# Kernel optimization log

Measured on AMD Instinct MI355X. Metric: run time of the kernel, lower is better.

## Reference

```python
import jax, jax.numpy as jnp
import numpy as np

B, T, E = 4, 2_000_000, 8
C, K, STRIDE = 128, 512, 512
CHUNK, OVERLAP = 64000, 511  # overlap defaults to kernel_size - 1


def _candidate_positions(T):
    """Exact set of window start positions visited by the chunked streaming max.

    Replays the chunk loop of _lowmem_max_over_time: chunk starts advance by
    step = chunk_size - overlap (not a multiple of stride!), and within each
    chunk conv windows start at chunk_start + stride*k.
    """
    step = max(1, CHUNK - OVERLAP)
    pos = []
    start = 0
    while start < T:
        end = min(start + CHUNK, T)
        end_ext = min(end + OVERLAP, T)
        L = end_ext - start
        if L >= K:
            n = (L - K) // STRIDE + 1
            pos.append(start + STRIDE * np.arange(n, dtype=np.int64))
        if end == T:
            break
        start += step
    p = np.unique(np.concatenate(pos))
    return np.clip(p, 0, max(0, T - K))


POS = _candidate_positions(T)                       # [P] static window starts
WIN_IDX = POS[:, None] + np.arange(K, dtype=np.int64)  # [P, K] gather indices


def setup_inputs() -> dict:
    key = jax.random.key(0)
    ks = jax.random.split(key, 5)
    scale = 1.0 / float(np.sqrt(E * K))  # torch Conv1d default init range
    return {
        "x": jax.random.normal(ks[0], (B, T, E), dtype=jnp.float32),
        "w1": jax.random.uniform(ks[1], (C, E, K), jnp.float32, -scale, scale),
        "b1": jax.random.uniform(ks[2], (C,), jnp.float32, -scale, scale),
        "w2": jax.random.uniform(ks[3], (C, E, K), jnp.float32, -scale, scale),
        "b2": jax.random.uniform(ks[4], (C,), jnp.float32, -scale, scale),
    }


def reference(x, w1, b1, w2, b2):
    # Gather every candidate window the chunked scan would see: [B, P, K, E]
    wins = x[:, WIN_IDX, :]
    # Original clones windows under no_grad (stop_grad_input=True): input gets no grad.
    wins = jax.lax.stop_gradient(wins)
    # Gated conv (GLU): conv1(z) * sigmoid(conv2(z)) at each window -> [B, C, P]
    c1 = jnp.einsum('bpke,cek->bcp', wins, w1) + b1[:, None]
    c2 = jnp.einsum('bpke,cek->bcp', wins, w2) + b2[:, None]
    g = c1 * jax.nn.sigmoid(c2)
    # Global max-over-time per (batch, channel); identical value to the
    # running-max pass followed by exact re-evaluation at argmax positions.
    return g.max(axis=-1)  # [B, C]
```

## Files before the change

kernel.cpp:

```cpp
#include <hip/hip_runtime.h>


#define T_LEN 2000000
#define P_CNT 3937
#define M_TOT 15748
#define KD    4096

typedef __attribute__((ext_vector_type(8))) short short8;
typedef __attribute__((ext_vector_type(4))) float f32x4;

static __device__ __forceinline__ unsigned short f2bf(float f) {
    unsigned u = __builtin_bit_cast(unsigned, f);
    unsigned r = (u + 0x7FFFu + ((u >> 16) & 1u)) >> 16;
    return (unsigned short)r;
}

static __device__ __forceinline__ unsigned ordenc(float f) {
    unsigned u = __builtin_bit_cast(unsigned, f);
    return (u & 0x80000000u) ? ~u : (u | 0x80000000u);
}

static __device__ __forceinline__ size_t row_base_bp(int bb, int p) {
    int j, kp;
    if (p < 3875) { j = p / 125; kp = p - j * 125; }
    else          { j = 31;      kp = p - 3875; }
    long pos = (long)j * 63489 + (long)kp * 512;
    return ((size_t)bb * T_LEN + (size_t)pos) * 8u;
}

static __device__ __forceinline__ uint2 cvt4(float4 v) {
    unsigned lo, hi;
    asm("v_cvt_pk_bf16_f32 %0, %1, %2" : "=v"(lo) : "v"(v.x), "v"(v.y));
    asm("v_cvt_pk_bf16_f32 %0, %1, %2" : "=v"(hi) : "v"(v.z), "v"(v.w));
    uint2 u; u.x = lo; u.y = hi;
    return u;
}

__global__ __launch_bounds__(256) void pack_w(const float* __restrict__ w1,
                                              const float* __restrict__ w2,
                                              uint4* __restrict__ Bpf,
                                              unsigned* __restrict__ outu) {
    int c = blockIdx.x * 256 + threadIdx.x;
    if (c < 512) outu[c] = 0u;
    if (c >= 131072) return;
    int l  = c & 63;
    int w  = (c >> 6) & 15;
    int kq = (c >> 10) & 1;
    int ks = c >> 11;
    int cl = l & 15;
    int n  = (cl < 8) ? (w * 8 + cl) : (128 + w * 8 + (cl - 8));
    int kb = ks * 64 + kq * 32 + ((l >> 4) << 3);
    const float* src = (n < 128) ? w1 : w2;
    int cc = n & 127;
    unsigned short h[8];
#pragma unroll
    for (int j = 0; j < 8; ++j) {
        int k = kb + j;
        h[j] = f2bf(src[cc * 4096 + (k & 7) * 512 + (k >> 3)]);
    }
    uint4 v;
    v.x = (unsigned)h[0] | ((unsigned)h[1] << 16);
    v.y = (unsigned)h[2] | ((unsigned)h[3] << 16);
    v.z = (unsigned)h[4] | ((unsigned)h[5] << 16);
    v.w = (unsigned)h[6] | ((unsigned)h[7] << 16);
    Bpf[c] = v;
}

#define LOAD_B(BB, KS)                                                         \
    do {                                                                       \
        _Pragma("unroll")                                                      \
        for (int kq = 0; kq < 2; ++kq)                                         \
            BB[kq] = Bq[((KS) * 2 + kq) * 1024 + bbase];                       \
    } while (0)

#define STEP_NB(KS, BCUR, BNXT)                                                \
    do {                                                                       \
        const int ks_ = (KS);                                                  \
        const int ksn = (ks_ + 1 < 64) ? ks_ + 1 : 63;                         \
        LOAD_B(BNXT, ksn);                                                     \
        const int ksl = (ks_ + 6 < 64) ? ks_ + 6 : 63;                         \
        float4 aF = *(const float4*)(x + aoff + (size_t)(ksl * 64));           \
        const char* As = smem + (ks_ & 7) * 8192;                              \
        _Pragma("unroll")                                                      \
        for (int kq = 0; kq < 2; ++kq) {                                       \
            short8 b = __builtin_bit_cast(short8, BCUR[kq]);                   \
            _Pragma("unroll")                                                  \
            for (int mf = 0; mf < 4; ++mf) {                                   \
                short8 af = *(const short8*)(As + aro[kq][mf]);                \
                acc[mf] = __builtin_amdgcn_mfma_f32_16x16x32_bf16(             \
                    af, b, acc[mf], 0, 0, 0);                                  \
            }                                                                  \
        }                                                                      \
        if (ks_ + 4 < 64)                                                      \
            *(uint2*)(smem + ((ks_ + 4) & 7) * 8192 + awb) = cvt4(aA);         \
        aA = aB; aB = aF;                                                      \
    } while (0)

__global__ __launch_bounds__(1024, 4) void gemm_max(const float* __restrict__ x,
                                                    const uint4* __restrict__ Bq,
                                                    const float* __restrict__ b1,
                                                    const float* __restrict__ b2,
                                                    unsigned* __restrict__ outu) {
    __shared__ __align__(16) char smem[65536];

    const int t    = threadIdx.x;
    const int lane = t & 63;
    const int w    = t >> 6;
    const int bid  = blockIdx.x;
    const int bb   = bid / 62;
    const int p0   = (bid % 62) * 64;

    const int rowS = t >> 4;
    const int kcS  = t & 15;
    int pS = p0 + rowS; if (pS > P_CNT - 1) pS = P_CNT - 1;
    const size_t aoff = row_base_bp(bb, pS) + (size_t)(kcS * 4);
    const int    awb  = (rowS * 128 + kcS * 8) ^ ((rowS & 7) << 4);

    int aro[2][4];
#pragma unroll
    for (int kq = 0; kq < 2; ++kq)
#pragma unroll
        for (int mf = 0; mf < 4; ++mf) {
            int row = mf * 16 + (lane & 15);
            aro[kq][mf] = (row * 128 + kq * 64 + (lane >> 4) * 16)
                          ^ ((row & 7) << 4);
        }

    const int bbase = w * 64 + lane;

#pragma unroll
    for (int pt = 0; pt < 4; ++pt) {
        float4 v = *(const float4*)(x + aoff + pt * 64);
        *(uint2*)(smem + pt * 8192 + awb) = cvt4(v);
    }
    __syncthreads();

    float4 aA = *(const float4*)(x + aoff + 256);
    float4 aB = *(const float4*)(x + aoff + 320);
    uint4 BX[2], BY[2];
    LOAD_B(BX, 0);

    f32x4 acc[4];
#pragma unroll
    for (int mf = 0; mf < 4; ++mf) acc[mf] = (f32x4){0.f, 0.f, 0.f, 0.f};

    for (int ks = 0; ks < 64; ks += 2) {
        STEP_NB(ks, BX, BY);
        STEP_NB(ks + 1, BY, BX);
        asm volatile("s_waitcnt lgkmcnt(15)" ::: "memory");
        __builtin_amdgcn_s_barrier();
        asm volatile("" ::: "memory");
    }

    const int   cidx = w * 8 + (lane & 7);
    const float bb1  = b1[cidx];
    const float bb2  = b2[cidx];
    float best = -3.4e38f;
#pragma unroll
    for (int mf = 0; mf < 4; ++mf)
#pragma unroll
        for (int q = 0; q < 4; ++q) {
            float v  = acc[mf][q];
            float ov = __shfl_xor(v, 8);
            float c1 = v + bb1;
            float c2 = ov + bb2;
            float g  = c1 / (1.f + __expf(-c2));
            best = fmaxf(best, g);
        }
    best = fmaxf(best, __shfl_xor(best, 16));
    best = fmaxf(best, __shfl_xor(best, 32));
    if (lane < 8)
        atomicMax(&outu[bb * 128 + w * 8 + lane], ordenc(best));
}

__global__ __launch_bounds__(256) void unmap_out(unsigned* __restrict__ outu) {
    int i = blockIdx.x * 256 + threadIdx.x;
    if (i < 512) {
        unsigned u = outu[i];
        outu[i] = (u & 0x80000000u) ? (u ^ 0x80000000u) : ~u;
    }
}

extern "C" void kernel_launch(void* const* d_in, const int* in_sizes, int n_in,
                              void* d_out, int out_size, void* d_ws, size_t ws_size,
                              hipStream_t stream) {
    const float* x  = (const float*)d_in[0];
    const float* w1 = (const float*)d_in[1];
    const float* b1 = (const float*)d_in[2];
    const float* w2 = (const float*)d_in[3];
    const float* b2 = (const float*)d_in[4];

    uint4*    Bpf  = (uint4*)d_ws;
    unsigned* outu = (unsigned*)d_out;

    pack_w<<<dim3(512), dim3(256), 0, stream>>>(w1, w2, Bpf, outu);

    const int nblk = 62 * 4;
    gemm_max<<<dim3(nblk), dim3(1024), 0, stream>>>(x, (const uint4*)Bpf, b1, b2, outu);

    unmap_out<<<dim3(2), dim3(256), 0, stream>>>(outu);
}
```

Before: 70.92 us.

## Split GEMM K dimension across two blocks and merge partials in separate kernel

The fused GEMM+GLU+max kernel is split-K: each block now handles half of the 4096-long reduction, doubling the grid from 248 to 496 blocks so the 256 CUs on the device are better covered. Partial accumulators are written to a workspace buffer, and a new merge kernel sums the two halves, applies bias and sigmoid gating, and takes the max with atomics. This trades an extra kernel launch plus partial-result write/read traffic (roughly 16 MB of fp32) for higher parallelism.

```diff
diff --git a/kernel.cpp b/kernel.cpp
--- a/kernel.cpp
+++ b/kernel.cpp
@@ -66,19 +66,19 @@
     Bpf[c] = v;
 }
 
-#define LOAD_B(BB, KS)                                                         \
+#define LOAD_B(BB, KT)                                                         \
     do {                                                                       \
         _Pragma("unroll")                                                      \
         for (int kq = 0; kq < 2; ++kq)                                         \
-            BB[kq] = Bq[((KS) * 2 + kq) * 1024 + bbase];                       \
+            BB[kq] = Bq[((KT) * 2 + kq) * 1024 + bbase];                       \
     } while (0)
 
 #define STEP_NB(KS, BCUR, BNXT)                                                \
     do {                                                                       \
         const int ks_ = (KS);                                                  \
-        const int ksn = (ks_ + 1 < 64) ? ks_ + 1 : 63;                         \
-        LOAD_B(BNXT, ksn);                                                     \
-        const int ksl = (ks_ + 6 < 64) ? ks_ + 6 : 63;                         \
+        const int ksn = (ks_ + 1 < 32) ? ks_ + 1 : 31;                         \
+        LOAD_B(BNXT, kbase + ksn);                                             \
+        const int ksl = (ks_ + 6 < 32) ? ks_ + 6 : 31;                         \
         float4 aF = *(const float4*)(x + aoff + (size_t)(ksl * 64));           \
         const char* As = smem + (ks_ & 7) * 8192;                              \
         _Pragma("unroll")                                                      \
@@ -91,29 +91,32 @@
                     af, b, acc[mf], 0, 0, 0);                                  \
             }                                                                  \
         }                                                                      \
-        if (ks_ + 4 < 64)                                                      \
+        if (ks_ + 4 < 32)                                                      \
             *(uint2*)(smem + ((ks_ + 4) & 7) * 8192 + awb) = cvt4(aA);         \
         aA = aB; aB = aF;                                                      \
     } while (0)
 
-__global__ __launch_bounds__(1024, 4) void gemm_max(const float* __restrict__ x,
-                                                    const uint4* __restrict__ Bq,
-                                                    const float* __restrict__ b1,
-                                                    const float* __restrict__ b2,
-                                                    unsigned* __restrict__ outu) {
+__global__ __launch_bounds__(1024, 8) void gemm_part(const float* __restrict__ x,
+                                                     const uint4* __restrict__ Bq,
+                                                     float* __restrict__ Cpart) {
     __shared__ __align__(16) char smem[65536];
 
     const int t    = threadIdx.x;
     const int lane = t & 63;
     const int w    = t >> 6;
     const int bid  = blockIdx.x;
-    const int bb   = bid / 62;
-    const int p0   = (bid % 62) * 64;
+    const int kh   = bid & 1;
+    const int rest = bid >> 1;
+    const int bb   = rest / 62;
+    const int mt   = rest % 62;
+    const int p0   = mt * 64;
+    const int kbase = kh * 32;
 
     const int rowS = t >> 4;
     const int kcS  = t & 15;
     int pS = p0 + rowS; if (pS > P_CNT - 1) pS = P_CNT - 1;
-    const size_t aoff = row_base_bp(bb, pS) + (size_t)(kcS * 4);
+    const size_t aoff = row_base_bp(bb, pS) + (size_t)(kcS * 4)
+                      + (size_t)kbase * 64;
     const int    awb  = (rowS * 128 + kcS * 8) ^ ((rowS & 7) << 4);
 
     int aro[2][4];
@@ -138,13 +141,13 @@
     float4 aA = *(const float4*)(x + aoff + 256);
     float4 aB = *(const float4*)(x + aoff + 320);
     uint4 BX[2], BY[2];
-    LOAD_B(BX, 0);
+    LOAD_B(BX, kbase);
 
     f32x4 acc[4];
 #pragma unroll
     for (int mf = 0; mf < 4; ++mf) acc[mf] = (f32x4){0.f, 0.f, 0.f, 0.f};
 
-    for (int ks = 0; ks < 64; ks += 2) {
+    for (int ks = 0; ks < 32; ks += 2) {
         STEP_NB(ks, BX, BY);
         STEP_NB(ks + 1, BY, BX);
         asm volatile("s_waitcnt lgkmcnt(15)" ::: "memory");
@@ -152,25 +155,47 @@
         asm volatile("" ::: "memory");
     }
 
-    const int   cidx = w * 8 + (lane & 7);
-    const float bb1  = b1[cidx];
-    const float bb2  = b2[cidx];
+    float* Cp = Cpart + (((size_t)(kh * 4 + bb) * 62 + mt) << 14);
+#pragma unroll
+    for (int mf = 0; mf < 4; ++mf)
+#pragma unroll
+        for (int q = 0; q < 4; ++q) {
+            int row = mf * 16 + (lane >> 4) * 4 + q;
+            Cp[row * 256 + w * 16 + (lane & 15)] = acc[mf][q];
+        }
+}
+
+__global__ __launch_bounds__(256) void merge_max(const float* __restrict__ Cpart,
+                                                 const float* __restrict__ b1,
+                                                 const float* __restrict__ b2,
+                                                 unsigned* __restrict__ outu) {
+    __shared__ float red[256];
+    const int bid = blockIdx.x;
+    const int bb  = bid / 62;
+    const int mt  = bid % 62;
+    const int t   = threadIdx.x;
+    const int c   = t & 127;
+    const int rh  = t >> 7;
+
+    const float* P0 = Cpart + (((size_t)(0 + bb) * 62 + mt) << 14);
+    const float* P1 = Cpart + (((size_t)(4 + bb) * 62 + mt) << 14);
+    const int v1 = (c >> 3) * 16 + (c & 7);
+    const int v2 = v1 + 8;
+    const float bb1 = b1[c];
+    const float bb2 = b2[c];
+
     float best = -3.4e38f;
-#pragma unroll
-    for (int mf = 0; mf < 4; ++mf)
-#pragma unroll
-        for (int q = 0; q < 4; ++q) {
-            float v  = acc[mf][q];
-            float ov = __shfl_xor(v, 8);
-            float c1 = v + bb1;
-            float c2 = ov + bb2;
-            float g  = c1 / (1.f + __expf(-c2));
-            best = fmaxf(best, g);
-        }
-    best = fmaxf(best, __shfl_xor(best, 16));
-    best = fmaxf(best, __shfl_xor(best, 32));
-    if (lane < 8)
-        atomicMax(&outu[bb * 128 + w * 8 + lane], ordenc(best));
+    for (int r = rh * 32; r < rh * 32 + 32; ++r) {
+        int o = r * 256;
+        float c1 = P0[o + v1] + P1[o + v1] + bb1;
+        float c2 = P0[o + v2] + P1[o + v2] + bb2;
+        float g  = c1 / (1.f + __expf(-c2));
+        best = fmaxf(best, g);
+    }
+    red[t] = best;
+    __syncthreads();
+    if (t < 128)
+        atomicMax(&outu[bb * 128 + c], ordenc(fmaxf(red[t], red[t + 128])));
 }
 
 __global__ __launch_bounds__(256) void unmap_out(unsigned* __restrict__ outu) {
@@ -190,13 +215,15 @@
     const float* w2 = (const float*)d_in[3];
     const float* b2 = (const float*)d_in[4];
 
-    uint4*    Bpf  = (uint4*)d_ws;
-    unsigned* outu = (unsigned*)d_out;
+    uint4*    Bpf   = (uint4*)d_ws;
+    float*    Cpart = (float*)((char*)d_ws + (2u << 20));
+    unsigned* outu  = (unsigned*)d_out;
 
     pack_w<<<dim3(512), dim3(256), 0, stream>>>(w1, w2, Bpf, outu);
 
-    const int nblk = 62 * 4;
-    gemm_max<<<dim3(nblk), dim3(1024), 0, stream>>>(x, (const uint4*)Bpf, b1, b2, outu);
+    gemm_part<<<dim3(496), dim3(1024), 0, stream>>>(x, (const uint4*)Bpf, Cpart);
+
+    merge_max<<<dim3(248), dim3(256), 0, stream>>>(Cpart, b1, b2, outu);
 
     unmap_out<<<dim3(2), dim3(256), 0, stream>>>(outu);
 }
```

New measurement: 91.02 us. 1.28x slower.
